# Optimization experiments

Measured on AMD Instinct MI355X. Metric: run time of the kernel, lower is better.

The kernel has to match this reference:

```python
import jax, jax.numpy as jnp
import numpy as np

B, K, H, W = 16, 32, 28, 28   # batch, set size, image h, image w
HID, OUT = 64, 64             # hid_dim, out_dim
NOPS = 8                      # permutation-equivariant 3->3 pool/broadcast basis ops


def setup_inputs() -> dict:
    key = jax.random.key(0)
    ks = jax.random.split(key, 8)
    def p(k, shape, fan_in):
        return jax.random.normal(k, shape, jnp.float32) / np.float32(np.sqrt(fan_in))
    return dict(
        x=jax.random.normal(ks[0], (B, K, H, W), jnp.float32),
        conv1_w=p(ks[1], (32, 1, 3, 3), 9),
        conv1_b=jnp.zeros((32,), jnp.float32),
        conv2_w=p(ks[2], (64, 32, 3, 3), 32 * 9),
        conv2_b=jnp.zeros((64,), jnp.float32),
        fc_w=p(ks[3], (HID, 64 * 7 * 7), 64 * 7 * 7),
        fc_b=jnp.zeros((HID,), jnp.float32),
        eq_w=p(ks[4], (HID, OUT, NOPS), HID * NOPS),
        eq_b=jnp.zeros((OUT,), jnp.float32),
        out_w=p(ks[5], (1, OUT), OUT),
        out_b=jnp.zeros((1,), jnp.float32),
    )


def _conv2d(x, w, b):
    y = jax.lax.conv_general_dilated(x, w, (1, 1), 'SAME',
                                     dimension_numbers=('NCHW', 'OIHW', 'NCHW'))
    return y + b[None, :, None, None]


def _maxpool2(x):
    return jax.lax.reduce_window(x, -jnp.inf, jax.lax.max,
                                 (1, 1, 2, 2), (1, 1, 2, 2), 'VALID')


def _forward(x, conv1_w, conv1_b, conv2_w, conv2_b, fc_w, fc_b, eq_w, eq_b, out_w, out_b):
    # --- BasicConvNet embed: (B*K, 1, H, W) -> (B*K, HID) ---
    x1 = x.reshape(B * K, 1, H, W)
    h1 = _maxpool2(jax.nn.relu(_conv2d(x1, conv1_w, conv1_b)))   # (B*K, 32, 14, 14)
    h2 = _maxpool2(jax.nn.relu(_conv2d(h1, conv2_w, conv2_b)))   # (B*K, 64, 7, 7)
    feat = jax.nn.relu(h2.reshape(B * K, -1) @ fc_w.T + fc_b)    # (B*K, HID)
    x4 = feat.reshape(B, K, HID)

    # --- triple outer product: (B, HID, K, K, K), no contracted index ---
    x5 = jnp.einsum('bid,bjd,bkd->bdijk', x4, x4, x4)

    # --- SetEq3to3: 8 equivariant pool/broadcast basis ops, contracted with eq_w[d,e,o].
    # Contract each pooled tensor with its slice of eq_w BEFORE broadcasting (same math,
    # avoids materializing 8 full (B,d,K,K,K) op tensors). ---
    m_i  = x5.mean(2)           # (B, d, j, k)
    m_j  = x5.mean(3)           # (B, d, i, k)
    m_k  = x5.mean(4)           # (B, d, i, j)
    m_ij = m_i.mean(2)          # (B, d, k)
    m_ik = m_i.mean(3)          # (B, d, j)
    m_jk = m_j.mean(3)          # (B, d, i)
    m_all = m_ij.mean(2)        # (B, d)

    x6 = (jnp.einsum('bdijk,de->beijk', x5, eq_w[:, :, 0])
          + jnp.einsum('bdjk,de->bejk', m_i, eq_w[:, :, 1])[:, :, None, :, :]
          + jnp.einsum('bdik,de->beik', m_j, eq_w[:, :, 2])[:, :, :, None, :]
          + jnp.einsum('bdij,de->beij', m_k, eq_w[:, :, 3])[:, :, :, :, None]
          + jnp.einsum('bdk,de->bek', m_ij, eq_w[:, :, 4])[:, :, None, None, :]
          + jnp.einsum('bdj,de->bej', m_ik, eq_w[:, :, 5])[:, :, None, :, None]
          + jnp.einsum('bdi,de->bei', m_jk, eq_w[:, :, 6])[:, :, :, None, None]
          + jnp.einsum('bd,de->be', m_all, eq_w[:, :, 7])[:, :, None, None, None]
          + eq_b[None, :, None, None, None])          # (B, OUT, K, K, K)

    # permute to channels-last, relu, pool over (i,j,k), relu, final linear
    x7 = jax.nn.relu(x6.transpose(0, 2, 3, 4, 1))     # (B, K, K, K, OUT)
    x8 = x7.mean(axis=(1, 2, 3))                      # (B, OUT)
    x9 = jax.nn.relu(x8)
    # dropout_prob = 0 -> identity
    return x9 @ out_w.T + out_b                       # (B, 1)


def reference(x, conv1_w, conv1_b, conv2_w, conv2_b, fc_w, fc_b, eq_w, eq_b, out_w, out_b):
    return _forward(x, conv1_w, conv1_b, conv2_w, conv2_b, fc_w, fc_b,
                    eq_w, eq_b, out_w, out_b)
```

## Files before the change

kernel.cpp:

```cpp
#include <hip/hip_runtime.h>
#include <hip/hip_bf16.h>


typedef __attribute__((ext_vector_type(8))) short short8;
typedef __attribute__((ext_vector_type(4))) float f32x4;

__device__ __forceinline__ f32x4 mfma_bf16(short8 a, short8 b, f32x4 c) {
  return __builtin_amdgcn_mfma_f32_16x16x32_bf16(a, b, c, 0, 0, 0);
}

__device__ __forceinline__ unsigned short f2bs(float f) {
  unsigned int u = __float_as_uint(f);
  unsigned int r = u + 0x7fffu + ((u >> 16) & 1u);
  return (unsigned short)(r >> 16);
}
__device__ __forceinline__ unsigned int pk2(float x, float y) {
  union { __hip_bfloat162 h; unsigned int u; } cv;
  cv.h = __float22bfloat162_rn(make_float2(x, y));
  return cv.u;
}
__device__ __forceinline__ void ub8(const short* p, float* f) {
  uint4 u = *(const uint4*)p;
  f[0] = __uint_as_float(u.x << 16); f[1] = __uint_as_float(u.x & 0xffff0000u);
  f[2] = __uint_as_float(u.y << 16); f[3] = __uint_as_float(u.y & 0xffff0000u);
  f[4] = __uint_as_float(u.z << 16); f[5] = __uint_as_float(u.z & 0xffff0000u);
  f[6] = __uint_as_float(u.w << 16); f[7] = __uint_as_float(u.w & 0xffff0000u);
}

__global__ __launch_bounds__(256) void k0_prep(const float* __restrict__ eqw,
    const float* __restrict__ w2, const float* __restrict__ fcw,
    float* __restrict__ W7t, short* __restrict__ Wtb,
    short* __restrict__ w2p, short* __restrict__ fcwt) {
  const int b = blockIdx.x, t = threadIdx.x;
  if (b < 8) {
    const int m = b;
    for (int idx = t; idx < 4096; idx += 256) {
      int e = idx >> 6, d = idx & 63;
      float v = eqw[d*512 + e*8 + m];
      if (m == 7) W7t[idx] = v;
      else        Wtb[m*4096 + idx] = (short)f2bs(v);
    }
  } else if (b == 8) {
    for (int idx = t; idx < 18432; idx += 256) {
      int s2 = idx & 7, c = (idx >> 3) & 63, quad = (idx >> 9) & 3, dd = idx >> 11;
      w2p[idx] = (short)f2bs(w2[c*288 + (quad*8 + s2)*9 + dd]);
    }
  } else {
    int base = (b - 9)*12544 + t;
    for (int q = 0; q < 49; ++q) {
      int idx = base + q*256;
      int k = idx >> 6, e = idx & 63;
      fcwt[idx] = (short)f2bs(fcw[e*3136 + k]);
    }
  }
}

__global__ __launch_bounds__(256, 2) void kA_conv(const float* __restrict__ x,
    const float* __restrict__ w1, const float* __restrict__ b1,
    const short* __restrict__ w2p, const float* __restrict__ b2,
    const short* __restrict__ fcwt, const float* __restrict__ fcb,
    float* __restrict__ feat) {
  const int n = blockIdx.x, t = threadIdx.x;
  __shared__ float si[30*30];
  __shared__ float sw[32*9];
  __shared__ float sb[32];
  __shared__ __align__(16) short inT[16*18*40];
  __shared__ __align__(16) float h2f[3136];
  __shared__ float sf4[256];
  const int wv = t >> 6, l = t & 63, quad = l >> 4, col = l & 15;

  const int c_out = wv*16 + col;
  short8 Bq[9];
  {
    const short8* wp = (const short8*)w2p + quad*64 + c_out;
#pragma unroll
    for (int dd = 0; dd < 9; ++dd) Bq[dd] = wp[dd*256];
  }
  const float bb2 = b2[c_out];

  for (int idx = t; idx < 900; idx += 256) si[idx] = 0.f;
  {
    unsigned int* zp = (unsigned int*)inT;
    for (int idx = t; idx < 5760; idx += 256) zp[idx] = 0u;
  }
  for (int idx = t; idx < 288; idx += 256) sw[idx] = w1[idx];
  if (t < 32) sb[t] = b1[t];
  __syncthreads();
  for (int idx = t; idx < 784; idx += 256) {
    int y = idx / 28, xx = idx - y*28;
    si[(y+1)*30 + xx + 1] = x[n*784 + idx];
  }
  __syncthreads();

  {
    const int cg = t & 7;
    float wreg[4][9], breg[4];
#pragma unroll
    for (int cc = 0; cc < 4; ++cc) {
      breg[cc] = sb[cg*4 + cc];
#pragma unroll
      for (int q = 0; q < 9; ++q) wreg[cc][q] = sw[(cg*4 + cc)*9 + q];
    }
    for (int idx = t; idx < 1568; idx += 256) {
      int pos = idx >> 3;
      int py = pos / 14, px = pos - py*14;
      float pt[4][4];
#pragma unroll
      for (int r = 0; r < 4; ++r)
#pragma unroll
        for (int q = 0; q < 4; ++q)
          pt[r][q] = si[(2*py + r)*30 + 2*px + q];
      float res[4];
#pragma unroll
      for (int cc = 0; cc < 4; ++cc) {
        float best = 0.f;
#pragma unroll
        for (int a = 0; a < 2; ++a)
#pragma unroll
          for (int b3 = 0; b3 < 2; ++b3) {
            float v = breg[cc]
              + wreg[cc][0]*pt[a+0][b3+0] + wreg[cc][1]*pt[a+0][b3+1] + wreg[cc][2]*pt[a+0][b3+2]
              + wreg[cc][3]*pt[a+1][b3+0] + wreg[cc][4]*pt[a+1][b3+1] + wreg[cc][5]*pt[a+1][b3+2]
              + wreg[cc][6]*pt[a+2][b3+0] + wreg[cc][7]*pt[a+2][b3+1] + wreg[cc][8]*pt[a+2][b3+2];
            best = fmaxf(best, v);
          }
        res[cc] = best;
      }
      uint2 pkd;
      pkd.x = pk2(res[0], res[1]);
      pkd.y = pk2(res[2], res[3]);
      *(uint2*)&inT[(py+1)*720 + (px+1)*40 + cg*4] = pkd;
    }
  }
  __syncthreads();

  for (int p = 0; p < 7; ++p) {
    short8 Ar[4][3];
#pragma unroll
    for (int rr = 0; rr < 4; ++rr)
#pragma unroll
      for (int dx = 0; dx < 3; ++dx)
        Ar[rr][dx] = *(const short8*)&inT[(2*p + rr)*720 + (col + dx)*40 + quad*8];
    f32x4 a0 = {0.f,0.f,0.f,0.f}, a1 = {0.f,0.f,0.f,0.f};
#pragma unroll
    for (int dy = 0; dy < 3; ++dy)
#pragma unroll
      for (int dx = 0; dx < 3; ++dx) {
        a0 = mfma_bf16(Ar[dy][dx],     Bq[dy*3 + dx], a0);
        a1 = mfma_bf16(Ar[dy + 1][dx], Bq[dy*3 + dx], a1);
      }
#pragma unroll
    for (int a = 0; a < 2; ++a) {
      int px = quad*2 + a;
      if (px < 7) {
        float m0 = fmaxf(fmaxf(a0[2*a], a0[2*a + 1]), fmaxf(a1[2*a], a1[2*a + 1]));
        h2f[c_out*49 + p*7 + px] = fmaxf(m0 + bb2, 0.f);
      }
    }
  }
  {
    const int g = l >> 3, s = l & 7;
    const short* Wp = fcwt + (wv*784 + g)*64 + s*8;
    const float* Hp = h2f + wv*784 + g;
    float acc[8] = {0.f,0.f,0.f,0.f,0.f,0.f,0.f,0.f};
#pragma unroll 7
    for (int j = 0; j < 98; ++j) {
      float wf[8]; ub8(Wp + j*512, wf);
      float hk = Hp[j*8];
#pragma unroll
      for (int q = 0; q < 8; ++q) acc[q] += wf[q] * hk;
    }
#pragma unroll
    for (int q = 0; q < 8; ++q) {
      acc[q] += __shfl_xor(acc[q], 8, 64);
      acc[q] += __shfl_xor(acc[q], 16, 64);
      acc[q] += __shfl_xor(acc[q], 32, 64);
    }
    if (g == 0) {
#pragma unroll
      for (int q = 0; q < 8; ++q) sf4[wv*64 + s*8 + q] = acc[q];
    }
  }
  __syncthreads();
  if (t < 64) {
    float v = sf4[t] + sf4[64 + t] + sf4[128 + t] + sf4[192 + t] + fcb[t];
    feat[n*64 + t] = fmaxf(v, 0.f);
  }
}

__global__ __launch_bounds__(256) void k4b(const float* __restrict__ feat,
    const float* __restrict__ W7t, const float* __restrict__ eqb,
    float* __restrict__ s, float* __restrict__ t7c) {
  __shared__ __align__(16) float sf[2048];
  __shared__ float ss[64];
  const int b = blockIdx.x, t = threadIdx.x;
  for (int v4 = t; v4 < 512; v4 += 256)
    *(float4*)&sf[v4*4] = *(const float4*)&feat[b*2048 + v4*4];
  __syncthreads();
  if (t < 64) {
    float a = 0.f;
#pragma unroll
    for (int r = 0; r < 32; ++r) a += sf[r*64 + t];
    a *= (1.f/32.f);
    s[b*64 + t] = a;
    ss[t] = a;
  }
  __syncthreads();
  if (t < 64) {
    const float* W7 = W7t + t*64;
    float t7 = 0.f;
    for (int d = 0; d < 64; ++d) {
      float sv = ss[d];
      t7 += sv*sv*sv * W7[d];
    }
    t7c[b*64 + t] = t7 + eqb[t];
  }
}

__global__ __launch_bounds__(256, 2) void k5_mfma(const float* __restrict__ feat,
    const float* __restrict__ s_, const short* __restrict__ Wtb,
    const float* __restrict__ t7c, float* __restrict__ x8p) {
  __shared__ __align__(16) float Fm[32*68];
  __shared__ __align__(16) float FI[64];
  __shared__ __align__(16) float SV[64];
  __shared__ __align__(16) float C0[64];
  __shared__ float C0P[128];
  __shared__ float KCf[32*68];
  __shared__ float JCf[32*68];
  __shared__ float RED[256];
  __shared__ __align__(16) short Fb[32*72];
  __shared__ __align__(16) short QPb[64*72];
  __shared__ __align__(16) short G2b[64*72];
  __shared__ __align__(16) short G3b[64*72];

  const int i = blockIdx.x, b = blockIdx.y, t = threadIdx.x;
  const int w = t >> 6, l = t & 63, quad = l >> 4, col = l & 15;

  for (int idx = t; idx < 2048; idx += 256) {
    int r = idx >> 6, d = idx & 63;
    float v = feat[b*2048 + idx];
    Fm[r*68 + d] = v;
    Fb[r*72 + d] = (short)f2bs(v);
  }
  if (t < 64) { FI[t] = feat[b*2048 + i*64 + t]; SV[t] = s_[b*64 + t]; }
  __syncthreads();

  {
    const int e = t >> 2, dbase = (t & 3) * 16;
#pragma unroll
    for (int h = 0; h < 2; ++h) {
      int off = dbase + h*8;
      float w0[8], w1[8], w2[8], w3[8], w4[8], w5[8];
      ub8(&Wtb[0*4096 + e*64 + off], w0);
      ub8(&Wtb[1*4096 + e*64 + off], w1);
      ub8(&Wtb[2*4096 + e*64 + off], w2);
      ub8(&Wtb[3*4096 + e*64 + off], w3);
      ub8(&Wtb[4*4096 + e*64 + off], w4);
      ub8(&Wtb[5*4096 + e*64 + off], w5);
      uint4 qv, g2v, g3v;
      unsigned int* qp = &qv.x;
      unsigned int* g2p = &g2v.x;
      unsigned int* g3p = &g3v.x;
#pragma unroll
      for (int j = 0; j < 4; ++j) {
        float fi0 = FI[off + 2*j],     fi1 = FI[off + 2*j + 1];
        float s0  = SV[off + 2*j],     s1  = SV[off + 2*j + 1];
        float q0 = fi0*w0[2*j]   + s0*w1[2*j];
        float q1 = fi1*w0[2*j+1] + s1*w1[2*j+1];
        float a0 = s0*(fi0*w2[2*j]   + s0*w4[2*j]);
        float a1 = s1*(fi1*w2[2*j+1] + s1*w4[2*j+1]);
        float c0 = s0*(fi0*w3[2*j]   + s0*w5[2*j]);
        float c1 = s1*(fi1*w3[2*j+1] + s1*w5[2*j+1]);
        qp[j]  = pk2(q0, q1);
        g2p[j] = pk2(a0, a1);
        g3p[j] = pk2(c0, c1);
      }
      *(uint4*)&QPb[e*72 + off] = qv;
      *(uint4*)&G2b[e*72 + off] = g2v;
      *(uint4*)&G3b[e*72 + off] = g3v;
    }
  }
  if (t < 128) {
    int e = t & 63, dh = t >> 6;
    const short* W6 = Wtb + 6*4096 + e*64 + dh*32;
    float a = 0.f;
#pragma unroll
    for (int g = 0; g < 4; ++g) {
      float wf[8];
      ub8(&W6[g*8], wf);
#pragma unroll
      for (int dd = 0; dd < 8; ++dd) {
        int d = dh*32 + g*8 + dd;
        float sd = SV[d];
        a += sd*sd*FI[d]*wf[dd];
      }
    }
    C0P[dh*64 + e] = a;
  }
  __syncthreads();

  if (w < 2) {
    const short* G = w ? G3b : G2b;
    float* DST = w ? JCf : KCf;
    short8 Bf[4][2];
#pragma unroll
    for (int n = 0; n < 4; ++n)
#pragma unroll
      for (int s2 = 0; s2 < 2; ++s2)
        Bf[n][s2] = *(const short8*)&G[(n*16 + col)*72 + s2*32 + quad*8];
#pragma unroll
    for (int m = 0; m < 2; ++m) {
      short8 A0 = *(const short8*)&Fb[(m*16 + col)*72 + quad*8];
      short8 A1 = *(const short8*)&Fb[(m*16 + col)*72 + 32 + quad*8];
#pragma unroll
      for (int n = 0; n < 4; ++n) {
        f32x4 z = {0.f, 0.f, 0.f, 0.f};
        f32x4 ac = mfma_bf16(A1, Bf[n][1], mfma_bf16(A0, Bf[n][0], z));
#pragma unroll
        for (int r = 0; r < 4; ++r)
          DST[(m*16 + quad*4 + r)*68 + n*16 + col] = ac[r];
      }
    }
  } else if (w == 2) {
    C0[l] = C0P[l] + C0P[64 + l] + t7c[b*64 + l];
  }
  __syncthreads();

  float c0v[4];
#pragma unroll
  for (int n = 0; n < 4; ++n) c0v[n] = C0[n*16 + col];
  float jcq[8][4];
#pragma unroll
  for (int jj = 0; jj < 8; ++jj)
#pragma unroll
    for (int n = 0; n < 4; ++n)
      jcq[jj][n] = JCf[(w*8 + jj)*68 + n*16 + col] + c0v[n];
  float kcv[2][4][4];
#pragma unroll
  for (int kb2 = 0; kb2 < 2; ++kb2)
#pragma unroll
    for (int r = 0; r < 4; ++r)
#pragma unroll
      for (int n = 0; n < 4; ++n)
        kcv[kb2][r][n] = KCf[(kb2*16 + quad*4 + r)*68 + n*16 + col];
  short8 Bq[4][2];
#pragma unroll
  for (int n = 0; n < 4; ++n)
#pragma unroll
    for (int s2 = 0; s2 < 2; ++s2)
      Bq[n][s2] = *(const short8*)&QPb[(n*16 + col)*72 + s2*32 + quad*8];

  float4 fkv[2][4];
#pragma unroll
  for (int kb2 = 0; kb2 < 2; ++kb2) {
    const float* fk = &Fm[(kb2*16 + col)*68 + quad*8];
    fkv[kb2][0] = *(const float4*)(fk);
    fkv[kb2][1] = *(const float4*)(fk + 4);
    fkv[kb2][2] = *(const float4*)(fk + 32);
    fkv[kb2][3] = *(const float4*)(fk + 36);
  }

  float sum[4] = {0.f, 0.f, 0.f, 0.f};
  union SU { short8 v; unsigned int u[4]; };

#pragma unroll
  for (int jj = 0; jj < 8; ++jj) {
    const float* fj = &Fm[(w*8 + jj)*68 + quad*8];
    float4 j0 = *(const float4*)(fj);
    float4 j1 = *(const float4*)(fj + 4);
    float4 j2 = *(const float4*)(fj + 32);
    float4 j3 = *(const float4*)(fj + 36);
#pragma unroll
    for (int kb2 = 0; kb2 < 2; ++kb2) {
      float4 k0 = fkv[kb2][0], k1 = fkv[kb2][1];
      float4 k2v = fkv[kb2][2], k3v = fkv[kb2][3];
      SU A0, A1;
      A0.u[0] = pk2(j0.x*k0.x, j0.y*k0.y);
      A0.u[1] = pk2(j0.z*k0.z, j0.w*k0.w);
      A0.u[2] = pk2(j1.x*k1.x, j1.y*k1.y);
      A0.u[3] = pk2(j1.z*k1.z, j1.w*k1.w);
      A1.u[0] = pk2(j2.x*k2v.x, j2.y*k2v.y);
      A1.u[1] = pk2(j2.z*k2v.z, j2.w*k2v.w);
      A1.u[2] = pk2(j3.x*k3v.x, j3.y*k3v.y);
      A1.u[3] = pk2(j3.z*k3v.z, j3.w*k3v.w);
      f32x4 ac[4];
#pragma unroll
      for (int n = 0; n < 4; ++n) {
        f32x4 z = {0.f, 0.f, 0.f, 0.f};
        ac[n] = mfma_bf16(A1.v, Bq[n][1], mfma_bf16(A0.v, Bq[n][0], z));
      }
#pragma unroll
      for (int n = 0; n < 4; ++n)
#pragma unroll
        for (int r = 0; r < 4; ++r) {
          float v = ac[n][r] + kcv[kb2][r][n] + jcq[jj][n];
          sum[n] += fmaxf(v, 0.f);
        }
    }
  }

#pragma unroll
  for (int n = 0; n < 4; ++n) {
    float v = sum[n];
    v += __shfl_xor(v, 16, 64);
    v += __shfl_xor(v, 32, 64);
    if (l < 16) RED[w*64 + n*16 + l] = v;
  }
  __syncthreads();
  if (t < 64) {
    float tot = RED[t] + RED[64 + t] + RED[128 + t] + RED[192 + t];
    x8p[(b*32 + i)*64 + t] = tot;
  }
}

__global__ __launch_bounds__(64) void k6_out(const float* __restrict__ x8p,
    const float* __restrict__ ow, const float* __restrict__ ob,
    float* __restrict__ out) {
  const int bb = blockIdx.x, t = threadIdx.x;
  float a = 0.f;
#pragma unroll
  for (int i = 0; i < 32; ++i) a += x8p[(bb*32 + i)*64 + t];
  float v = fmaxf(a * (1.f/32768.f), 0.f) * ow[t];
#pragma unroll
  for (int off = 32; off > 0; off >>= 1) v += __shfl_down(v, off, 64);
  if (t == 0) out[bb] = v + ob[0];
}

extern "C" void kernel_launch(void* const* d_in, const int* in_sizes, int n_in,
                              void* d_out, int out_size, void* d_ws, size_t ws_size,
                              hipStream_t stream) {
  const float* x   = (const float*)d_in[0];
  const float* c1w = (const float*)d_in[1];
  const float* c1b = (const float*)d_in[2];
  const float* c2w = (const float*)d_in[3];
  const float* c2b = (const float*)d_in[4];
  const float* fcw = (const float*)d_in[5];
  const float* fcb = (const float*)d_in[6];
  const float* eqw = (const float*)d_in[7];
  const float* eqb = (const float*)d_in[8];
  const float* ow  = (const float*)d_in[9];
  const float* ob  = (const float*)d_in[10];
  float* out = (float*)d_out;

  float* feat = (float*)d_ws;
  float* x8p  = feat + 32768;
  float* W7t  = x8p + 32768;
  short* Wtb  = (short*)(W7t + 4096);
  short* w2p  = Wtb + 28672;
  short* fcwt = w2p + 18432;
  float* s    = (float*)(fcwt + 200704);
  float* t7c  = s + 1024;
  (void)in_sizes; (void)n_in; (void)out_size; (void)ws_size;

  hipLaunchKernelGGL(k0_prep, dim3(25), dim3(256), 0, stream,
                     eqw, c2w, fcw, W7t, Wtb, w2p, fcwt);
  hipLaunchKernelGGL(kA_conv, dim3(512), dim3(256), 0, stream,
                     x, c1w, c1b, w2p, c2b, fcwt, fcb, feat);
  hipLaunchKernelGGL(k4b,     dim3(16),  dim3(256), 0, stream,
                     feat, W7t, eqb, s, t7c);
  hipLaunchKernelGGL(k5_mfma, dim3(32, 16), dim3(256), 0, stream,
                     feat, s, Wtb, t7c, x8p);
  hipLaunchKernelGGL(k6_out,  dim3(16),  dim3(64),  0, stream, x8p, ow, ob, out);
}
```

Measured before the change: 127.2 us.

## Fuse set-mean into conv via atomics, fold t7 into k5, parallelize weight prep

New measurement: 124.7 us. About the same (-1.9%).

```diff
diff --git a/kernel.cpp b/kernel.cpp
--- a/kernel.cpp
+++ b/kernel.cpp
@@ -30,7 +30,7 @@
 __global__ __launch_bounds__(256) void k0_prep(const float* __restrict__ eqw,
     const float* __restrict__ w2, const float* __restrict__ fcw,
     float* __restrict__ W7t, short* __restrict__ Wtb,
-    short* __restrict__ w2p, short* __restrict__ fcwt) {
+    short* __restrict__ w2p, short* __restrict__ fcwt, float* __restrict__ s) {
   const int b = blockIdx.x, t = threadIdx.x;
   if (b < 8) {
     const int m = b;
@@ -41,16 +41,30 @@
       else        Wtb[m*4096 + idx] = (short)f2bs(v);
     }
   } else if (b == 8) {
-    for (int idx = t; idx < 18432; idx += 256) {
+    for (int idx = t; idx < 1024; idx += 256) s[idx] = 0.f;
+  } else if (b < 13) {
+    const int base = (b - 9)*4608;
+#pragma unroll
+    for (int q = 0; q < 18; ++q) {
+      int idx = base + q*256 + t;
       int s2 = idx & 7, c = (idx >> 3) & 63, quad = (idx >> 9) & 3, dd = idx >> 11;
       w2p[idx] = (short)f2bs(w2[c*288 + (quad*8 + s2)*9 + dd]);
     }
   } else {
-    int base = (b - 9)*12544 + t;
-    for (int q = 0; q < 49; ++q) {
-      int idx = base + q*256;
-      int k = idx >> 6, e = idx & 63;
-      fcwt[idx] = (short)f2bs(fcw[e*3136 + k]);
+    __shared__ short tile[64][65];
+    const int j = b - 13;
+    const int kk = t & 63, eb = t >> 6;
+#pragma unroll
+    for (int p = 0; p < 16; ++p) {
+      int e = p*4 + eb;
+      tile[e][kk] = (short)f2bs(fcw[e*3136 + j*64 + kk]);
+    }
+    __syncthreads();
+    const int e = t & 63, kb = t >> 6;
+#pragma unroll
+    for (int p = 0; p < 16; ++p) {
+      int k = p*4 + kb;
+      fcwt[(j*64 + k)*64 + e] = tile[e][k];
     }
   }
 }
@@ -59,7 +73,7 @@
     const float* __restrict__ w1, const float* __restrict__ b1,
     const short* __restrict__ w2p, const float* __restrict__ b2,
     const short* __restrict__ fcwt, const float* __restrict__ fcb,
-    float* __restrict__ feat) {
+    float* __restrict__ feat, float* __restrict__ s) {
   const int n = blockIdx.x, t = threadIdx.x;
   __shared__ float si[30*30];
   __shared__ float sw[32*9];
@@ -159,8 +173,8 @@
     }
   }
   {
-    const int g = l >> 3, s = l & 7;
-    const short* Wp = fcwt + (wv*784 + g)*64 + s*8;
+    const int g = l >> 3, s2 = l & 7;
+    const short* Wp = fcwt + (wv*784 + g)*64 + s2*8;
     const float* Hp = h2f + wv*784 + g;
     float acc[8] = {0.f,0.f,0.f,0.f,0.f,0.f,0.f,0.f};
 #pragma unroll 7
@@ -178,48 +192,22 @@
     }
     if (g == 0) {
 #pragma unroll
-      for (int q = 0; q < 8; ++q) sf4[wv*64 + s*8 + q] = acc[q];
+      for (int q = 0; q < 8; ++q) sf4[wv*64 + s2*8 + q] = acc[q];
     }
   }
   __syncthreads();
   if (t < 64) {
     float v = sf4[t] + sf4[64 + t] + sf4[128 + t] + sf4[192 + t] + fcb[t];
-    feat[n*64 + t] = fmaxf(v, 0.f);
-  }
-}
-
-__global__ __launch_bounds__(256) void k4b(const float* __restrict__ feat,
-    const float* __restrict__ W7t, const float* __restrict__ eqb,
-    float* __restrict__ s, float* __restrict__ t7c) {
-  __shared__ __align__(16) float sf[2048];
-  __shared__ float ss[64];
-  const int b = blockIdx.x, t = threadIdx.x;
-  for (int v4 = t; v4 < 512; v4 += 256)
-    *(float4*)&sf[v4*4] = *(const float4*)&feat[b*2048 + v4*4];
-  __syncthreads();
-  if (t < 64) {
-    float a = 0.f;
-#pragma unroll
-    for (int r = 0; r < 32; ++r) a += sf[r*64 + t];
-    a *= (1.f/32.f);
-    s[b*64 + t] = a;
-    ss[t] = a;
-  }
-  __syncthreads();
-  if (t < 64) {
-    const float* W7 = W7t + t*64;
-    float t7 = 0.f;
-    for (int d = 0; d < 64; ++d) {
-      float sv = ss[d];
-      t7 += sv*sv*sv * W7[d];
-    }
-    t7c[b*64 + t] = t7 + eqb[t];
+    v = fmaxf(v, 0.f);
+    feat[n*64 + t] = v;
+    atomicAdd(&s[(n >> 5)*64 + t], v * (1.f/32.f));
   }
 }
 
 __global__ __launch_bounds__(256, 2) void k5_mfma(const float* __restrict__ feat,
     const float* __restrict__ s_, const short* __restrict__ Wtb,
-    const float* __restrict__ t7c, float* __restrict__ x8p) {
+    const float* __restrict__ W7t, const float* __restrict__ eqb,
+    float* __restrict__ x8p) {
   __shared__ __align__(16) float Fm[32*68];
   __shared__ __align__(16) float FI[64];
   __shared__ __align__(16) float SV[64];
@@ -322,7 +310,14 @@
       }
     }
   } else if (w == 2) {
-    C0[l] = C0P[l] + C0P[64 + l] + t7c[b*64 + l];
+    const float* W7 = W7t + l*64;
+    float t7 = 0.f;
+#pragma unroll 8
+    for (int d = 0; d < 64; ++d) {
+      float sv = SV[d];
+      t7 += sv*sv*sv * W7[d];
+    }
+    C0[l] = C0P[l] + C0P[64 + l] + t7 + eqb[l];
   }
   __syncthreads();
 
@@ -449,16 +444,13 @@
   short* w2p  = Wtb + 28672;
   short* fcwt = w2p + 18432;
   float* s    = (float*)(fcwt + 200704);
-  float* t7c  = s + 1024;
   (void)in_sizes; (void)n_in; (void)out_size; (void)ws_size;
 
-  hipLaunchKernelGGL(k0_prep, dim3(25), dim3(256), 0, stream,
-                     eqw, c2w, fcw, W7t, Wtb, w2p, fcwt);
+  hipLaunchKernelGGL(k0_prep, dim3(62), dim3(256), 0, stream,
+                     eqw, c2w, fcw, W7t, Wtb, w2p, fcwt, s);
   hipLaunchKernelGGL(kA_conv, dim3(512), dim3(256), 0, stream,
-                     x, c1w, c1b, w2p, c2b, fcwt, fcb, feat);
-  hipLaunchKernelGGL(k4b,     dim3(16),  dim3(256), 0, stream,
-                     feat, W7t, eqb, s, t7c);
+                     x, c1w, c1b, w2p, c2b, fcwt, fcb, feat, s);
   hipLaunchKernelGGL(k5_mfma, dim3(32, 16), dim3(256), 0, stream,
-                     feat, s, Wtb, t7c, x8p);
+                     feat, s, Wtb, W7t, eqb, x8p);
   hipLaunchKernelGGL(k6_out,  dim3(16),  dim3(64),  0, stream, x8p, ow, ob, out);
 }
```
